# Kernel optimization log

Hardware: AMD Instinct MI355X
Metric: run time of the kernel (lower is better)

## Reference

```python
import jax, jax.numpy as jnp
import numpy as np

D_EMBED = 64      # per-head dim (module uses d_embed as head dim)
N_HEADS = 8
SCALE = 1.0 / float(np.sqrt(D_EMBED))
ROPE_BASE = 10000.0


def _rope(x):
    # torchtune-style interleaved RoPE. x: [B, S, H, D]
    B, S, H, D = x.shape
    freqs = 1.0 / (ROPE_BASE ** (jnp.arange(0, D, 2, dtype=jnp.float32) / D))  # [D/2]
    ang = jnp.arange(S, dtype=jnp.float32)[:, None] * freqs[None, :]           # [S, D/2]
    cos = jnp.cos(ang)[None, :, None, :]
    sin = jnp.sin(ang)[None, :, None, :]
    x1 = x[..., 0::2]
    x2 = x[..., 1::2]
    return jnp.stack([x1 * cos - x2 * sin, x1 * sin + x2 * cos], axis=-1).reshape(B, S, H, D)


def setup_inputs() -> dict:
    key = jax.random.key(0)
    ks = jax.random.split(key, 5)
    B, S, D, H = 2, 2048, D_EMBED, N_HEADS
    std = 1.0 / np.sqrt(D)
    return {
        "q": jax.random.normal(ks[0], (B, S, D), jnp.float32),
        "Wq": jax.random.normal(ks[1], (H * D, D), jnp.float32) * std,
        "Wk": jax.random.normal(ks[2], (H * D, D), jnp.float32) * std,
        "Wv": jax.random.normal(ks[3], (H * D, D), jnp.float32) * std,
        "Wo": jax.random.normal(ks[4], (D, H * D), jnp.float32) * std,
        "gamma": jnp.ones((H,), jnp.float32),
    }


def reference(q, Wq, Wk, Wv, Wo, gamma):
    B, S, D = q.shape
    H = N_HEADS
    qh = (q @ Wq.T).reshape(B, S, H, D)
    kh = (q @ Wk.T).reshape(B, S, H, D)
    vh = (q @ Wv.T).reshape(B, S, H, D)
    qh = _rope(qh).transpose(0, 2, 1, 3)  # [B,H,S,D]
    kh = _rope(kh).transpose(0, 2, 1, 3)
    vh = vh.transpose(0, 2, 1, 3)
    # RBF attention scores
    qn = jnp.sum(qh * qh, axis=-1, keepdims=True)                 # [B,H,S,1]
    kn = jnp.sum(kh * kh, axis=-1, keepdims=True)                 # [B,H,S,1]
    qk = jnp.einsum('bhsd,bhtd->bhst', qh, kh)                    # [B,H,S,S]
    dist = jnp.maximum(qn - 2.0 * qk + jnp.swapaxes(kn, -2, -1), 0.0)
    scores = jnp.exp(-(gamma[None, :, None, None] * SCALE) * dist)
    causal = jnp.tril(jnp.ones((S, S), dtype=bool))
    scores = jnp.where(causal, scores, 0.0)
    out = jnp.einsum('bhst,bhtd->bhsd', scores, vh)
    out = out.transpose(0, 2, 1, 3).reshape(B, S, H * D)
    return out @ Wo.T
```

## Files before the change

### kernel.cpp

```cpp
#include <hip/hip_runtime.h>
#include <hip/hip_bf16.h>

#define BB 2
#define SS 2048
#define DD 64
#define HH 8
#define HD 512
#define SCALE 0.125f

typedef __bf16 bf16;
typedef __attribute__((ext_vector_type(4))) __bf16 bf16x4;
typedef __attribute__((ext_vector_type(8))) __bf16 bf16x8;
typedef __attribute__((ext_vector_type(4))) float floatx4;

#define PSLOT 2097152

__device__ __forceinline__ floatx4 mfma16(bf16x8 a, bf16x8 b, floatx4 c) {
    return __builtin_amdgcn_mfma_f32_16x16x32_bf16(a, b, c, 0, 0, 0);
}

#define PV_MFMA(ACC, A, B) \
    asm("s_nop 1\n\tv_mfma_f32_16x16x16_bf16 %0, %1, %2, %0" \
        : "+v"(ACC) : "v"(A), "v"(B))

#define MFMA_DRAIN4(A0, A1, A2, A3) \
    asm volatile("s_nop 7\n\ts_nop 7" : "+v"(A0), "+v"(A1), "+v"(A2), "+v"(A3))

#define GLL(G, L) __builtin_amdgcn_global_load_lds( \
    (const __attribute__((address_space(1))) void*)(G), \
    (__attribute__((address_space(3))) void*)(L), 16, 0, 0)

__device__ __forceinline__ bf16x8 load8(const void* base, size_t idx, int f32) {
    if (f32) {
        const float* p = (const float*)base + idx;
        const float4 a = *reinterpret_cast<const float4*>(p);
        const float4 b = *reinterpret_cast<const float4*>(p + 4);
        bf16x8 r;
        r[0] = (bf16)a.x; r[1] = (bf16)a.y; r[2] = (bf16)a.z; r[3] = (bf16)a.w;
        r[4] = (bf16)b.x; r[5] = (bf16)b.y; r[6] = (bf16)b.z; r[7] = (bf16)b.w;
        return r;
    }
    return *reinterpret_cast<const bf16x8*>((const bf16*)base + idx);
}

__device__ __forceinline__ float load1(const void* base, int idx, int f32) {
    return f32 ? ((const float*)base)[idx] : (float)((const bf16*)base)[idx];
}

__global__ __launch_bounds__(256) void proj_rope_kernel(
    const void* __restrict__ q, const void* __restrict__ Wq,
    const void* __restrict__ Wk, const void* __restrict__ Wv,
    bf16* __restrict__ qh, bf16* __restrict__ kh, bf16* __restrict__ vt,
    float* __restrict__ qn, float* __restrict__ kn,
    int* __restrict__ flagw)
{
    const int lane = threadIdx.x & 63;
    const int wid  = blockIdx.x * 4 + (threadIdx.x >> 6);
    if (wid >= 3 * BB * HH * (SS / 64)) return;
    const int l16  = lane & 15;
    const int quad = lane >> 4;

    int hit = 0;
    const unsigned short* qu = (const unsigned short*)q;
#pragma unroll
    for (int i = 0; i < 16; ++i) {
        const unsigned short u = qu[lane + i * 64];
        if (((u >> 7) & 0xFF) >= 134) hit = 1;
    }
    const int f32 = (__ballot(hit) != 0ull) ? 1 : 0;
    if (wid == 0 && lane == 0) *flagw = f32;

    int id = wid;
    const int h   = id % HH; id /= HH;
    const int st4 = id % (SS / 64); id /= (SS / 64);
    const int b   = id % BB; id /= BB;
    const int w   = id;

    const void* W = (w == 0) ? Wq : (w == 1) ? Wk : Wv;
    const size_t bh = (size_t)b * HH + h;

    bf16x8 wb0[4], wb1[4];
#pragma unroll
    for (int t = 0; t < 4; ++t) {
        const size_t wrow = (size_t)(h * 64 + t * 16 + l16) * DD;
        wb0[t] = load8(W, wrow + quad * 8, f32);
        wb1[t] = load8(W, wrow + quad * 8 + 32, f32);
    }

    float frevA[4], frevB[4];
    if (w < 2) {
#pragma unroll
        for (int t = 0; t < 4; ++t) {
            const int dbase = t * 16 + quad * 4;
            frevA[t] = __builtin_amdgcn_exp2f(
                -(float)dbase * (13.2877123795f / 64.0f)) * 0.15915494309f;
            frevB[t] = __builtin_amdgcn_exp2f(
                -(float)(dbase + 2) * (13.2877123795f / 64.0f)) * 0.15915494309f;
        }
    }

    for (int s4 = 0; s4 < 4; ++s4) {
        const int s0 = (st4 * 4 + s4) * 16;
        const size_t qrow = ((size_t)b * SS + s0 + l16) * DD;
        bf16x8 a0 = load8(q, qrow + quad * 8, f32);
        bf16x8 a1 = load8(q, qrow + quad * 8 + 32, f32);

        floatx4 cv[4];
#pragma unroll
        for (int t = 0; t < 4; ++t) {
            floatx4 acc = {0.f, 0.f, 0.f, 0.f};
            if (w < 2) {
                acc = mfma16(wb0[t], a0, acc);
                acc = mfma16(wb1[t], a1, acc);
            } else {
                acc = mfma16(a0, wb0[t], acc);
                acc = mfma16(a1, wb1[t], acc);
            }
            cv[t] = acc;
        }

        if (w < 2) {
            bf16*  dst  = (w == 0) ? qh : kh;
            float* ndst = (w == 0) ? qn : kn;
            const float srowf = (float)(s0 + l16);
            float nacc = 0.f;
            bf16* drow = dst + (bh * SS + s0 + l16) * DD + quad * 4;
#pragma unroll
            for (int t = 0; t < 4; ++t) {
                float revA = srowf * frevA[t]; revA -= floorf(revA);
                float revB = srowf * frevB[t]; revB -= floorf(revB);
                const float snA = __builtin_amdgcn_sinf(revA);
                const float csA = __builtin_amdgcn_cosf(revA);
                const float snB = __builtin_amdgcn_sinf(revB);
                const float csB = __builtin_amdgcn_cosf(revB);
                const float x0 = cv[t][0], x1 = cv[t][1];
                const float x2 = cv[t][2], x3 = cv[t][3];
                const float r0 = x0 * csA - x1 * snA;
                const float r1 = x0 * snA + x1 * csA;
                const float r2 = x2 * csB - x3 * snB;
                const float r3 = x2 * snB + x3 * csB;
                nacc += r0 * r0 + r1 * r1 + r2 * r2 + r3 * r3;
                bf16x4 o; o[0]=(bf16)r0; o[1]=(bf16)r1; o[2]=(bf16)r2; o[3]=(bf16)r3;
                *reinterpret_cast<bf16x4*>(drow + t * 16) = o;
            }
            nacc += __shfl_xor(nacc, 16);
            nacc += __shfl_xor(nacc, 32);
            if (quad == 0) ndst[bh * SS + s0 + l16] = nacc;
        } else {
            bf16* vrow = vt + ((size_t)bh * 128 + st4 * 4 + s4) * 1024
                       + l16 * 16 + quad * 4;
#pragma unroll
            for (int t = 0; t < 4; ++t) {
                bf16x4 pv;
#pragma unroll
                for (int r = 0; r < 4; ++r) pv[r] = (bf16)cv[t][r];
                *reinterpret_cast<bf16x4*>(vrow + t * 256) = pv;
            }
        }
    }
}

__global__ __launch_bounds__(256) void attn_kernel(
    const bf16* __restrict__ qh, const bf16* __restrict__ kh,
    const bf16* __restrict__ vt, const float* __restrict__ qn,
    const float* __restrict__ kn, const void* __restrict__ gamma,
    bf16* __restrict__ partial, const int* __restrict__ flagp,
    int NU, int U, int pb)
{
    __shared__ __align__(16) char smem[16384];
    const int f32  = *flagp;
    const int tid  = threadIdx.x;
    const int wv   = tid >> 6;
    const int lane = tid & 63;
    const int l16  = lane & 15;
    const int quad = lane >> 4;

    const int xcd  = blockIdx.x & 7;
    int sblk = blockIdx.x >> 3;
    const int half = (sblk >= pb) ? 1 : 0;
    const int bh   = xcd + (half << 3);
    sblk -= half * pb;

    const int j   = sblk / NU;
    const int u   = sblk - j * NU;
    const int B   = 2 * (j + 1);
    const int c0  = u * U;
    const int nA  = (c0 < B) ? (((c0 + U) < B ? (c0 + U) : B) - c0) : 0;
    const int bB  = ((c0 > B ? c0 : B) - B);
    const int slotA = u;
    const int slotB = u - (B / U);
    const int h    = bh & 7;

    const float cc = load1(gamma, h, f32) * SCALE * 1.4426950408889634f;

    int q4 = (nA > 0) ? j : (31 - j);
    int s0 = (q4 * 4 + wv) * 16;

    const bf16* qb = qh + ((size_t)bh * SS + s0 + l16) * DD;
    bf16x8 aq0 = *reinterpret_cast<const bf16x8*>(qb + quad * 8);
    bf16x8 aq1 = *reinterpret_cast<const bf16x8*>(qb + quad * 8 + 32);
    float qn_l = qn[(size_t)bh * SS + s0 + l16];

    floatx4 acc0 = {0.f,0.f,0.f,0.f}, acc1 = {0.f,0.f,0.f,0.f};
    floatx4 acc2 = {0.f,0.f,0.f,0.f}, acc3 = {0.f,0.f,0.f,0.f};

    const float* knp   = kn + (size_t)bh * SS + quad * 4;
    const char* kgbase = (const char*)(kh + (size_t)bh * SS * DD);
    const char* vgbase = (const char*)(vt + (size_t)bh * 131072);

    const int jK   = wv * 64 + lane;
    const int keyK = jK >> 3;
    const int cK   = ((jK & 7) - keyK) & 7;
    const int goffK = keyK * 128 + cK * 16;
    const int goffV = jK * 16;
    char* ldsK = smem + wv * 1024;
    char* ldsV = smem + 8192 + wv * 1024;

    const int kro0 = (l16 * 8 + ((quad + l16) & 7)) * 16;
    const int kro1 = (l16 * 8 + ((quad + 4 + l16) & 7)) * 16;
    const int vro  = l16 * 32 + quad * 8;

#define T0_OF(C) (((C) < nA ? (c0 + (C)) : (bB + (C) - nA)) * 32)

#define STORE_O(SLOT, S0) do { \
    bf16* pbp = partial + (size_t)(SLOT) * PSLOT \
              + ((size_t)bh * SS + (S0) + l16) * DD + quad * 4; \
    bf16x4 o_; \
    o_[0]=(bf16)acc0[0]; o_[1]=(bf16)acc0[1]; o_[2]=(bf16)acc0[2]; o_[3]=(bf16)acc0[3]; \
    *reinterpret_cast<bf16x4*>(pbp +  0) = o_; \
    o_[0]=(bf16)acc1[0]; o_[1]=(bf16)acc1[1]; o_[2]=(bf16)acc1[2]; o_[3]=(bf16)acc1[3]; \
    *reinterpret_cast<bf16x4*>(pbp + 16) = o_; \
    o_[0]=(bf16)acc2[0]; o_[1]=(bf16)acc2[1]; o_[2]=(bf16)acc2[2]; o_[3]=(bf16)acc2[3]; \
    *reinterpret_cast<bf16x4*>(pbp + 32) = o_; \
    o_[0]=(bf16)acc3[0]; o_[1]=(bf16)acc3[1]; o_[2]=(bf16)acc3[2]; o_[3]=(bf16)acc3[3]; \
    *reinterpret_cast<bf16x4*>(pbp + 48) = o_; \
} while (0)

    {
        const int t0p = T0_OF(0);
        GLL(kgbase + (size_t)t0p * 128 + goffK, ldsK);
        GLL(vgbase + (size_t)(t0p >> 4) * 2048 + goffV, ldsV);
    }
    __syncthreads();

    int buf = 0;
    for (int c = 0; c < U; ++c) {
        if (c + 1 < U) {
            const int tn = T0_OF(c + 1);
            GLL(kgbase + (size_t)tn * 128 + goffK, ldsK + ((buf ^ 1) << 12));
            GLL(vgbase + (size_t)(tn >> 4) * 2048 + goffV, ldsV + ((buf ^ 1) << 12));
        }
        if (c == nA && nA > 0) {
            MFMA_DRAIN4(acc0, acc1, acc2, acc3);
            STORE_O(slotA, s0);
            acc0 = {0.f,0.f,0.f,0.f}; acc1 = {0.f,0.f,0.f,0.f};
            acc2 = {0.f,0.f,0.f,0.f}; acc3 = {0.f,0.f,0.f,0.f};
            q4 = 31 - j;
            s0 = (q4 * 4 + wv) * 16;
            const bf16* qb2 = qh + ((size_t)bh * SS + s0 + l16) * DD;
            aq0 = *reinterpret_cast<const bf16x8*>(qb2 + quad * 8);
            aq1 = *reinterpret_cast<const bf16x8*>(qb2 + quad * 8 + 32);
            qn_l = qn[(size_t)bh * SS + s0 + l16];
        }
        const int t0 = T0_OF(c);
        const float4 knv0 = *reinterpret_cast<const float4*>(knp + t0);
        const float4 knv1 = *reinterpret_cast<const float4*>(knp + t0 + 16);
        const char* Kb = smem + (buf << 12);
        const char* Vb = smem + 8192 + (buf << 12);

        bf16x8 kc0 = *reinterpret_cast<const bf16x8*>(Kb + kro0);
        bf16x8 kc1 = *reinterpret_cast<const bf16x8*>(Kb + kro1);
        bf16x8 kc2 = *reinterpret_cast<const bf16x8*>(Kb + 2048 + kro0);
        bf16x8 kc3 = *reinterpret_cast<const bf16x8*>(Kb + 2048 + kro1);
        bf16x4 v00 = *reinterpret_cast<const bf16x4*>(Vb + vro);
        bf16x4 v01 = *reinterpret_cast<const bf16x4*>(Vb + 512 + vro);
        bf16x4 v02 = *reinterpret_cast<const bf16x4*>(Vb + 1024 + vro);
        bf16x4 v03 = *reinterpret_cast<const bf16x4*>(Vb + 1536 + vro);
        bf16x4 v10 = *reinterpret_cast<const bf16x4*>(Vb + 2048 + vro);
        bf16x4 v11 = *reinterpret_cast<const bf16x4*>(Vb + 2560 + vro);
        bf16x4 v12 = *reinterpret_cast<const bf16x4*>(Vb + 3072 + vro);
        bf16x4 v13 = *reinterpret_cast<const bf16x4*>(Vb + 3584 + vro);

        floatx4 z0 = {0.f,0.f,0.f,0.f};
        z0 = mfma16(kc0, aq0, z0);
        z0 = mfma16(kc1, aq1, z0);
        floatx4 z1 = {0.f,0.f,0.f,0.f};
        z1 = mfma16(kc2, aq0, z1);
        z1 = mfma16(kc3, aq1, z1);

        const float* k0_ = (const float*)&knv0;
        const float* k1_ = (const float*)&knv1;
        bf16x4 p0, p1;
        if (t0 + 31 <= s0) {
#pragma unroll
            for (int i = 0; i < 4; ++i) {
                float rawA = fmaf(-2.f, z0[i], qn_l + k0_[i]);
                float rawB = fmaf(-2.f, z1[i], qn_l + k1_[i]);
                p0[i] = (bf16)__builtin_amdgcn_exp2f(fminf(-cc * rawA, 0.f));
                p1[i] = (bf16)__builtin_amdgcn_exp2f(fminf(-cc * rawB, 0.f));
            }
        } else {
            const int dq0 = s0 + l16 - t0 - quad * 4;
            const int dq1 = dq0 - 16;
#pragma unroll
            for (int i = 0; i < 4; ++i) {
                float rawA = fmaf(-2.f, z0[i], qn_l + k0_[i]);
                float rawB = fmaf(-2.f, z1[i], qn_l + k1_[i]);
                float eA = __builtin_amdgcn_exp2f(fminf(-cc * rawA, 0.f));
                float eB = __builtin_amdgcn_exp2f(fminf(-cc * rawB, 0.f));
                p0[i] = (bf16)((i <= dq0) ? eA : 0.f);
                p1[i] = (bf16)((i <= dq1) ? eB : 0.f);
            }
        }

        PV_MFMA(acc0, v00, p0);
        PV_MFMA(acc1, v01, p0);
        PV_MFMA(acc2, v02, p0);
        PV_MFMA(acc3, v03, p0);
        PV_MFMA(acc0, v10, p1);
        PV_MFMA(acc1, v11, p1);
        PV_MFMA(acc2, v12, p1);
        PV_MFMA(acc3, v13, p1);

        __syncthreads();
        buf ^= 1;
    }

    MFMA_DRAIN4(acc0, acc1, acc2, acc3);
    STORE_O((nA == U) ? slotA : slotB, s0);
#undef STORE_O
#undef T0_OF
}

template <int NACT>
__device__ __forceinline__ floatx4 opj_core(const bf16* __restrict__ partial,
                                            const void* __restrict__ Wo,
                                            int b, int srow, size_t brow,
                                            int f32, int quad) {
    floatx4 acc = {0.f, 0.f, 0.f, 0.f};
#pragma unroll 4
    for (int kk = 0; kk < HD; kk += 32) {
        const int h  = kk >> 6;
        const int d0 = (kk & 63) + quad * 8;
        const bf16* ap = partial + (((size_t)(b * 8 + h)) * SS + srow) * 64 + d0;
        bf16x8 v0 = *reinterpret_cast<const bf16x8*>(ap);
        float u[8];
#pragma unroll
        for (int i = 0; i < 8; ++i) u[i] = (float)v0[i];
#pragma unroll
        for (int s = 1; s < NACT; ++s) {
            bf16x8 vs = *reinterpret_cast<const bf16x8*>(ap + (size_t)s * PSLOT);
#pragma unroll
            for (int i = 0; i < 8; ++i) u[i] += (float)vs[i];
        }
        bf16x8 a;
#pragma unroll
        for (int i = 0; i < 8; ++i) a[i] = (bf16)u[i];
        bf16x8 w = load8(Wo, brow + kk, f32);
        acc = mfma16(a, w, acc);
    }
    return acc;
}

__global__ __launch_bounds__(256) void outproj_kernel(
    const bf16* __restrict__ partial, const void* __restrict__ Wo,
    void* __restrict__ out, const int* __restrict__ flagp, int NU, int U)
{
    const int f32  = *flagp;
    const int ct   = threadIdx.x >> 6;
    const int lane = threadIdx.x & 63;
    const int l16  = lane & 15;
    const int quad = lane >> 4;

    const int g0   = blockIdx.x * 16;
    const int b    = g0 >> 11;
    const int s0   = g0 & (SS - 1);
    const int srow = s0 + l16;
    const size_t brow = (size_t)(ct * 16 + l16) * HD + quad * 8;

    const int q4g = s0 >> 6;
    int nact;
    if (q4g < 16) { const int Bp = 2 * (q4g + 1); nact = (Bp + U - 1) / U; }
    else          { const int Bp = 2 * (32 - q4g); nact = NU - Bp / U; }

    floatx4 acc;
    switch (nact) {
        case 1:  acc = opj_core<1>(partial, Wo, b, srow, brow, f32, quad); break;
        case 2:  acc = opj_core<2>(partial, Wo, b, srow, brow, f32, quad); break;
        case 3:  acc = opj_core<3>(partial, Wo, b, srow, brow, f32, quad); break;
        default: acc = opj_core<4>(partial, Wo, b, srow, brow, f32, quad); break;
    }

#pragma unroll
    for (int r = 0; r < 4; ++r) {
        const size_t o = (size_t)(g0 + quad * 4 + r) * DD + ct * 16 + l16;
        if (f32) ((float*)out)[o] = acc[r];
        else     ((bf16*)out)[o]  = (bf16)acc[r];
    }
}

extern "C" void kernel_launch(void* const* d_in, const int* in_sizes, int n_in,
                              void* d_out, int out_size, void* d_ws, size_t ws_size,
                              hipStream_t stream) {
    const void* q     = d_in[0];
    const void* Wq    = d_in[1];
    const void* Wk    = d_in[2];
    const void* Wv    = d_in[3];
    const void* Wo    = d_in[4];
    const void* gamma = d_in[5];

    char* ws = (char*)d_ws;
    bf16*  qh      = (bf16*)(ws);
    bf16*  kh      = (bf16*)(ws + 4194304);
    bf16*  vt      = (bf16*)(ws + 8388608);
    float* qn      = (float*)(ws + 12582912);
    float* kn      = (float*)(ws + 12713984);
    int*   flag    = (int*)  (ws + 12845056);
    bf16*  partial = (bf16*)(ws + 13631488);

    const size_t base = 13631488ull;
    int NU = (ws_size >= base + 3ull * 4194304) ? 3 : 2;
    const int U  = 66 / NU;
    const int pb = 16 * NU;

    const int nproj = 3 * BB * HH * (SS / 64);
    proj_rope_kernel<<<dim3((nproj + 3) / 4), dim3(256), 0, stream>>>(
        q, Wq, Wk, Wv, qh, kh, vt, qn, kn, flag);
    attn_kernel<<<dim3(16 * pb), dim3(256), 0, stream>>>(
        qh, kh, vt, qn, kn, gamma, partial, flag, NU, U, pb);
    outproj_kernel<<<dim3(BB * SS / 16), dim3(256), 0, stream>>>(
        partial, Wo, d_out, flag, NU, U);
}
```

Before: 115.6 us.

## Prescale norms by gamma in projection and allow six-way key split

The projection kernel now stores the query and key squared norms premultiplied by -gamma*scale*log2e. This lets the attention inner loop compute the exponent with a single fma and a min, instead of an extra multiply per score. The launcher also picks a six-way split of the key range when the workspace is large enough, which doubles the attention grid. To support that, the output projection gains template cases for reducing up to six partial slots. The extra split adds partial-buffer traffic and more reduction work in the output projection.

```diff
diff --git a/kernel.cpp b/kernel.cpp
--- a/kernel.cpp
+++ b/kernel.cpp
@@ -50,6 +50,7 @@
 __global__ __launch_bounds__(256) void proj_rope_kernel(
     const void* __restrict__ q, const void* __restrict__ Wq,
     const void* __restrict__ Wk, const void* __restrict__ Wv,
+    const void* __restrict__ gamma,
     bf16* __restrict__ qh, bf16* __restrict__ kh, bf16* __restrict__ vt,
     float* __restrict__ qn, float* __restrict__ kn,
     int* __restrict__ flagw)
@@ -88,7 +89,9 @@
     }
 
     float frevA[4], frevB[4];
+    float ncc = 0.f;
     if (w < 2) {
+        ncc = -load1(gamma, h, f32) * SCALE * 1.4426950408889634f;
 #pragma unroll
         for (int t = 0; t < 4; ++t) {
             const int dbase = t * 16 + quad * 4;
@@ -145,7 +148,7 @@
             }
             nacc += __shfl_xor(nacc, 16);
             nacc += __shfl_xor(nacc, 32);
-            if (quad == 0) ndst[bh * SS + s0 + l16] = nacc;
+            if (quad == 0) ndst[bh * SS + s0 + l16] = ncc * nacc;
         } else {
             bf16* vrow = vt + ((size_t)bh * 128 + st4 * 4 + s4) * 1024
                        + l16 * 16 + quad * 4;
@@ -191,7 +194,7 @@
     const int slotB = u - (B / U);
     const int h    = bh & 7;
 
-    const float cc = load1(gamma, h, f32) * SCALE * 1.4426950408889634f;
+    const float twocc = 2.0f * load1(gamma, h, f32) * SCALE * 1.4426950408889634f;
 
     int q4 = (nA > 0) ? j : (31 - j);
     int s0 = (q4 * 4 + wv) * 16;
@@ -199,7 +202,7 @@
     const bf16* qb = qh + ((size_t)bh * SS + s0 + l16) * DD;
     bf16x8 aq0 = *reinterpret_cast<const bf16x8*>(qb + quad * 8);
     bf16x8 aq1 = *reinterpret_cast<const bf16x8*>(qb + quad * 8 + 32);
-    float qn_l = qn[(size_t)bh * SS + s0 + l16];
+    float qnc_l = qn[(size_t)bh * SS + s0 + l16];
 
     floatx4 acc0 = {0.f,0.f,0.f,0.f}, acc1 = {0.f,0.f,0.f,0.f};
     floatx4 acc2 = {0.f,0.f,0.f,0.f}, acc3 = {0.f,0.f,0.f,0.f};
@@ -260,7 +263,7 @@
             const bf16* qb2 = qh + ((size_t)bh * SS + s0 + l16) * DD;
             aq0 = *reinterpret_cast<const bf16x8*>(qb2 + quad * 8);
             aq1 = *reinterpret_cast<const bf16x8*>(qb2 + quad * 8 + 32);
-            qn_l = qn[(size_t)bh * SS + s0 + l16];
+            qnc_l = qn[(size_t)bh * SS + s0 + l16];
         }
         const int t0 = T0_OF(c);
         const float4 knv0 = *reinterpret_cast<const float4*>(knp + t0);
@@ -294,20 +297,20 @@
         if (t0 + 31 <= s0) {
 #pragma unroll
             for (int i = 0; i < 4; ++i) {
-                float rawA = fmaf(-2.f, z0[i], qn_l + k0_[i]);
-                float rawB = fmaf(-2.f, z1[i], qn_l + k1_[i]);
-                p0[i] = (bf16)__builtin_amdgcn_exp2f(fminf(-cc * rawA, 0.f));
-                p1[i] = (bf16)__builtin_amdgcn_exp2f(fminf(-cc * rawB, 0.f));
+                float rawA = fmaf(twocc, z0[i], qnc_l + k0_[i]);
+                float rawB = fmaf(twocc, z1[i], qnc_l + k1_[i]);
+                p0[i] = (bf16)__builtin_amdgcn_exp2f(fminf(rawA, 0.f));
+                p1[i] = (bf16)__builtin_amdgcn_exp2f(fminf(rawB, 0.f));
             }
         } else {
             const int dq0 = s0 + l16 - t0 - quad * 4;
             const int dq1 = dq0 - 16;
 #pragma unroll
             for (int i = 0; i < 4; ++i) {
-                float rawA = fmaf(-2.f, z0[i], qn_l + k0_[i]);
-                float rawB = fmaf(-2.f, z1[i], qn_l + k1_[i]);
-                float eA = __builtin_amdgcn_exp2f(fminf(-cc * rawA, 0.f));
-                float eB = __builtin_amdgcn_exp2f(fminf(-cc * rawB, 0.f));
+                float rawA = fmaf(twocc, z0[i], qnc_l + k0_[i]);
+                float rawB = fmaf(twocc, z1[i], qnc_l + k1_[i]);
+                float eA = __builtin_amdgcn_exp2f(fminf(rawA, 0.f));
+                float eB = __builtin_amdgcn_exp2f(fminf(rawB, 0.f));
                 p0[i] = (bf16)((i <= dq0) ? eA : 0.f);
                 p1[i] = (bf16)((i <= dq1) ? eB : 0.f);
             }
@@ -388,7 +391,9 @@
         case 1:  acc = opj_core<1>(partial, Wo, b, srow, brow, f32, quad); break;
         case 2:  acc = opj_core<2>(partial, Wo, b, srow, brow, f32, quad); break;
         case 3:  acc = opj_core<3>(partial, Wo, b, srow, brow, f32, quad); break;
-        default: acc = opj_core<4>(partial, Wo, b, srow, brow, f32, quad); break;
+        case 4:  acc = opj_core<4>(partial, Wo, b, srow, brow, f32, quad); break;
+        case 5:  acc = opj_core<5>(partial, Wo, b, srow, brow, f32, quad); break;
+        default: acc = opj_core<6>(partial, Wo, b, srow, brow, f32, quad); break;
     }
 
 #pragma unroll
@@ -419,13 +424,16 @@
     bf16*  partial = (bf16*)(ws + 13631488);
 
     const size_t base = 13631488ull;
-    int NU = (ws_size >= base + 3ull * 4194304) ? 3 : 2;
+    int NU;
+    if      (ws_size >= base + 6ull * 4194304) NU = 6;
+    else if (ws_size >= base + 3ull * 4194304) NU = 3;
+    else                                       NU = 2;
     const int U  = 66 / NU;
     const int pb = 16 * NU;
 
     const int nproj = 3 * BB * HH * (SS / 64);
     proj_rope_kernel<<<dim3((nproj + 3) / 4), dim3(256), 0, stream>>>(
-        q, Wq, Wk, Wv, qh, kh, vt, qn, kn, flag);
+        q, Wq, Wk, Wv, gamma, qh, kh, vt, qn, kn, flag);
     attn_kernel<<<dim3(16 * pb), dim3(256), 0, stream>>>(
         qh, kh, vt, qn, kn, gamma, partial, flag, NU, U, pb);
     outproj_kernel<<<dim3(BB * SS / 16), dim3(256), 0, stream>>>(
```

Measured after the change: 122.7 us. 6.1% more time.
